# Optimization experiments

Measured on AMD Instinct MI355X. Metric: run time of the kernel, lower is better.

Reference implementation:

```python
import jax, jax.numpy as jnp
import numpy as np

DIM = 768
HEADS = 8
HEAD_DIM = DIM // HEADS  # 96, divisible by 6 for 3-axis RoPE
ROPE_BASE = 10000.0


def rotary_pe_3d(x, coords):
    """Apply 3D-coordinate rotary embedding.
    x: [B, h, L, d] with d % 6 == 0; coords: [B, L, 3].
    Head dim is split into 3 equal blocks, one per spatial axis; each block
    gets rotate-half RoPE with angle = coord_axis * inv_freq.
    """
    B, h, L, d = x.shape
    d3 = d // 3
    half = d3 // 2
    inv_freq = 1.0 / (ROPE_BASE ** (jnp.arange(half, dtype=x.dtype) / half))  # [half]
    ang = coords[..., None] * inv_freq  # [B, L, 3, half]
    cos = jnp.cos(ang)[:, None]  # [B, 1, L, 3, half]
    sin = jnp.sin(ang)[:, None]
    xr = x.reshape(B, h, L, 3, d3)
    x1, x2 = xr[..., :half], xr[..., half:]
    out = jnp.concatenate([x1 * cos - x2 * sin, x1 * sin + x2 * cos], axis=-1)
    return out.reshape(B, h, L, d)


def setup_inputs() -> dict:
    key = jax.random.key(0)
    ks = jax.random.split(key, 9)
    B, Lq, Lk = 2, 2048, 2048
    s = DIM ** -0.5
    return {
        "Q_in": jax.random.normal(ks[0], (B, Lq, DIM), jnp.float32),
        "K_in": jax.random.normal(ks[1], (B, Lk, DIM), jnp.float32),
        "V_in": jax.random.normal(ks[2], (B, Lk, DIM), jnp.float32),
        "coords_q": jax.random.uniform(ks[3], (B, Lq, 3), jnp.float32) * 10.0,
        "coords_k": jax.random.uniform(ks[4], (B, Lk, 3), jnp.float32) * 10.0,
        "Wq": jax.random.normal(ks[5], (DIM, DIM), jnp.float32) * s,
        "Wk": jax.random.normal(ks[6], (DIM, DIM), jnp.float32) * s,
        "Wv": jax.random.normal(ks[7], (DIM, DIM), jnp.float32) * s,
        "Wo": jax.random.normal(ks[8], (DIM, DIM), jnp.float32) * s,
    }


def _split_heads(x, h):
    B, L, C = x.shape
    return x.reshape(B, L, h, C // h).transpose(0, 2, 1, 3)  # [B,h,L,d]


def reference(Q_in, K_in, V_in, coords_q, coords_k, Wq, Wk, Wv, Wo):
    scale = HEAD_DIM ** -0.5
    q = _split_heads(Q_in @ Wq.T, HEADS)
    k = _split_heads(K_in @ Wk.T, HEADS)
    v = _split_heads(V_in @ Wv.T, HEADS)
    q = rotary_pe_3d(q, coords_q)
    k = rotary_pe_3d(k, coords_k)
    attn = jnp.einsum('bhqd,bhkd->bhqk', q, k) * scale
    attn = jax.nn.softmax(attn, axis=-1)
    out = jnp.einsum('bhqk,bhkd->bhqd', attn, v)
    B, h, L, d = out.shape
    out = out.transpose(0, 2, 1, 3).reshape(B, L, h * d)
    return out @ Wo.T
```

## Files before the change

kernel.cpp:

```cpp
#include <hip/hip_runtime.h>
#include <stdint.h>

#define H 8
#define DH 96
#define L 2048
#define NB 2
#define D 768

typedef unsigned short u16;
typedef unsigned int u32;
typedef __attribute__((ext_vector_type(4))) __bf16 bf16x4;
typedef __attribute__((ext_vector_type(8))) __bf16 bf16x8;
typedef __attribute__((ext_vector_type(4))) float f32x4;
typedef __attribute__((ext_vector_type(16))) float f32x16;
typedef __attribute__((ext_vector_type(4))) u32 u32x4;
typedef __attribute__((ext_vector_type(2))) u32 u32x2;
typedef __attribute__((ext_vector_type(4))) u16 u16x4;

#define QSCALE 0.14724444f

static __device__ __forceinline__ u16 f2bf(float f) {
  union { __bf16 h; u16 u; } v;
  v.h = (__bf16)f;
  return v.u;
}

static __device__ __forceinline__ bf16x8 cvt8r(f32x4 a, f32x4 b) {
  bf16x8 r;
  r[0] = (__bf16)a[0]; r[1] = (__bf16)a[1]; r[2] = (__bf16)a[2]; r[3] = (__bf16)a[3];
  r[4] = (__bf16)b[0]; r[5] = (__bf16)b[1]; r[6] = (__bf16)b[2]; r[7] = (__bf16)b[3];
  return r;
}

__global__ __launch_bounds__(256, 3)
void proj_qkv(const float* __restrict__ Qin, const float* __restrict__ Kin,
              const float* __restrict__ Vin,
              const float* __restrict__ Wq, const float* __restrict__ Wk,
              const float* __restrict__ Wv,
              const float* __restrict__ cq, const float* __restrict__ ck,
              u16* __restrict__ qo, u16* __restrict__ ko, u16* __restrict__ vo)
{
  __shared__ u16 a_lds[2][64 * 40];
  __shared__ u16 b_lds[2][192 * 40];
  const int tid = threadIdx.x;
  const int lane = tid & 63;
  const int w = tid >> 6;
  const int wr = w >> 1, wc = w & 1;
  const int fr = lane & 15;
  const int hi = lane >> 4;

  const int f = blockIdx.x;
  const int xcd = f & 7;
  const int g = f >> 3;
  const int bx = g & 3;
  const int h2 = g >> 2;
  const int byp = h2 & 7;
  const int z = h2 >> 3;
  const int by = xcd + 8 * byp;
  const int row0 = by * 64;
  const int col0 = bx * 192;

  const float* A = (z == 0) ? Qin : ((z == 1) ? Kin : Vin);
  const float* W = (z == 0) ? Wq : ((z == 1) ? Wk : Wv);

  const int arow = tid >> 2;
  const int acol = (tid & 3) * 8;
  const float* pA = A + (size_t)(row0 + arow) * D + acol;
  const float* pB0 = W + (size_t)(col0 + arow) * D + acol;
  const float* pB1 = pB0 + (size_t)64 * D;
  const float* pB2 = pB0 + (size_t)128 * D;

  f32x4 acc[2][6] = {};
  f32x4 Ra[2], Rb[6];

  auto issue = [&](int k) {
    Ra[0] = *(const f32x4*)(pA + k);
    Ra[1] = *(const f32x4*)(pA + k + 4);
    Rb[0] = *(const f32x4*)(pB0 + k);
    Rb[1] = *(const f32x4*)(pB0 + k + 4);
    Rb[2] = *(const f32x4*)(pB1 + k);
    Rb[3] = *(const f32x4*)(pB1 + k + 4);
    Rb[4] = *(const f32x4*)(pB2 + k);
    Rb[5] = *(const f32x4*)(pB2 + k + 4);
  };
  auto stage = [&](int bi) {
    *(bf16x8*)(&a_lds[bi][arow * 40 + acol]) = cvt8r(Ra[0], Ra[1]);
    *(bf16x8*)(&b_lds[bi][arow * 40 + acol]) = cvt8r(Rb[0], Rb[1]);
    *(bf16x8*)(&b_lds[bi][(arow + 64) * 40 + acol]) = cvt8r(Rb[2], Rb[3]);
    *(bf16x8*)(&b_lds[bi][(arow + 128) * 40 + acol]) = cvt8r(Rb[4], Rb[5]);
  };
  auto compute = [&](int bi) {
    bf16x8 af[2], bf[6];
#pragma unroll
    for (int m = 0; m < 2; m++)
      af[m] = *(const bf16x8*)(&a_lds[bi][(wr * 32 + m * 16 + fr) * 40 + hi * 8]);
#pragma unroll
    for (int n = 0; n < 6; n++)
      bf[n] = *(const bf16x8*)(&b_lds[bi][(wc * 96 + n * 16 + fr) * 40 + hi * 8]);
#pragma unroll
    for (int m = 0; m < 2; m++)
#pragma unroll
      for (int n = 0; n < 6; n++)
        acc[m][n] = __builtin_amdgcn_mfma_f32_16x16x32_bf16(af[m], bf[n], acc[m][n], 0, 0, 0);
  };

  issue(0);
  stage(0);
  __syncthreads();

  int cur = 0;
#pragma unroll 1
  for (int t = 0; t < 24; t++) {
    if (t + 1 < 24) issue((t + 1) * 32);
    compute(cur);
    if (t + 1 < 24) stage(cur ^ 1);
    __syncthreads();
    cur ^= 1;
  }

  const int hh = (col0 + wc * 96) / DH;
  if (z == 2) {
#pragma unroll
    for (int m = 0; m < 2; m++) {
      int rbase = row0 + wr * 32 + m * 16 + hi * 4;
#pragma unroll
      for (int n = 0; n < 6; n++) {
        int dd = n * 16 + fr;
#pragma unroll
        for (int r = 0; r < 4; r++) {
          int row = rbase + r;
          int b = row >> 11, l = row & (L - 1);
          vo[((size_t)((b * H + hh) * DH + dd)) * L + l] = f2bf(acc[m][n][r]);
        }
      }
    }
  } else {
    const float* coords = (z == 0) ? cq : ck;
    u16* outp = (z == 0) ? qo : ko;
    const float postscale = (z == 0) ? QSCALE : 1.0f;
    const float invf = exp2f(-(float)fr * 0.83048202372184058f);
#pragma unroll
    for (int m = 0; m < 2; m++) {
      int rbase = row0 + wr * 32 + m * 16 + hi * 4;
#pragma unroll
      for (int np = 0; np < 3; np++) {
        int n1 = np * 2;
        int dd1 = n1 * 16 + fr;
#pragma unroll
        for (int r = 0; r < 4; r++) {
          int row = rbase + r;
          int b = row >> 11, l = row & (L - 1);
          float coord = coords[((size_t)(b * L + l)) * 3 + np];
          float ang = coord * invf;
          float sn = __sinf(ang), cs = __cosf(ang);
          float x1 = acc[m][n1][r], x2 = acc[m][n1 + 1][r];
          size_t base = ((size_t)((b * H + hh) * L + l)) * DH;
          outp[base + dd1] = f2bf((x1 * cs - x2 * sn) * postscale);
          outp[base + dd1 + 16] = f2bf((x1 * sn + x2 * cs) * postscale);
        }
      }
    }
  }
}

#define KSTR 104
#define VSTR 76
#define NT   (L / 64)
__global__ __launch_bounds__(256, 2)
void attn_fwd(const u16* __restrict__ q_ws, const u16* __restrict__ k_ws,
              const u16* __restrict__ vt_ws, u16* __restrict__ ao)
{
  __shared__ __attribute__((aligned(16))) u16 k_lds[2][64 * KSTR];
  __shared__ __attribute__((aligned(16))) u16 vt_lds[2][96 * VSTR];
  const int tid = threadIdx.x;
  const int lane = tid & 63;
  const int w = tid >> 6;

  const int f = blockIdx.x;
  const int xr = f & 7;
  const int g = f >> 3;
  const int qx = g & 31;
  const int bh = xr + 8 * (g >> 5);
  const int q0 = qx * 64;

  const int qlo = lane & 31;
  const int hi32 = lane >> 5;
  const int wq = w >> 1;
  const int kk0 = (w & 1) * 32;

  const u16* kbase = k_ws + (size_t)bh * L * DH;
  const u16* vtbase = vt_ws + (size_t)bh * DH * L;

  const int perm[4] = {0, 2, 1, 3};

  int kg_off[3], kl0[3], kl1[3];
  int vg_off[3], vl0[3], vl1[3];
#pragma unroll
  for (int it = 0; it < 3; it++) {
    int ch = tid + it * 256;
    int krow = ch / 12, dc = ch % 12;
    kg_off[it] = krow * DH + dc * 8;
    int c0 = dc * 2;
    kl0[it] = krow * KSTR + (c0 >> 2) * 16 + perm[c0 & 3] * 4;
    kl1[it] = krow * KSTR + (c0 >> 2) * 16 + perm[(c0 + 1) & 3] * 4;
    int vrow = ch >> 3, vq = (ch & 7) * 2;
    vg_off[it] = vrow * L + vq * 4;
    vl0[it] = vrow * VSTR + (vq >> 2) * 16 + perm[vq & 3] * 4;
    vl1[it] = vrow * VSTR + (vq >> 2) * 16 + perm[(vq + 1) & 3] * 4;
  }

  bf16x8 qf[6];
  {
    const u16* qb = q_ws + ((size_t)bh * L + q0 + wq * 32 + qlo) * DH;
#pragma unroll
    for (int s = 0; s < 6; s++) {
      bf16x4 a = *(const bf16x4*)(qb + s * 16 + hi32 * 4);
      bf16x4 b = *(const bf16x4*)(qb + s * 16 + hi32 * 4 + 8);
      bf16x8 q;
      q[0] = a[0]; q[1] = a[1]; q[2] = a[2]; q[3] = a[3];
      q[4] = b[0]; q[5] = b[1]; q[6] = b[2]; q[7] = b[3];
      qf[s] = q;
    }
  }

  f32x16 o[3] = {};
  float m_r = -1e30f, l_r = 0.f;

  u32x4 kreg[3], vreg[3];
  auto kissue = [&](int t) {
    const u16* kb = kbase + (size_t)t * 64 * DH;
    const u16* vb = vtbase + t * 64;
#pragma unroll
    for (int it = 0; it < 3; it++) {
      kreg[it] = *(const u32x4*)(kb + kg_off[it]);
      vreg[it] = *(const u32x4*)(vb + vg_off[it]);
    }
  };
  auto kwrite = [&](int bi) {
#pragma unroll
    for (int it = 0; it < 3; it++) {
      u32x2 klo = { kreg[it][0], kreg[it][1] };
      u32x2 khi = { kreg[it][2], kreg[it][3] };
      *(u32x2*)(&k_lds[bi][kl0[it]]) = klo;
      *(u32x2*)(&k_lds[bi][kl1[it]]) = khi;
      u32x2 vlo = { vreg[it][0], vreg[it][1] };
      u32x2 vhi = { vreg[it][2], vreg[it][3] };
      *(u32x2*)(&vt_lds[bi][vl0[it]]) = vlo;
      *(u32x2*)(&vt_lds[bi][vl1[it]]) = vhi;
    }
  };

  kissue(0);
  kwrite(0);
  __syncthreads();

  int cur = 0;
  for (int t = 0; t < NT; t++) {
    if (t + 1 < NT) kissue(t + 1);

    f32x16 s2 = {};
#pragma unroll
    for (int s = 0; s < 6; s++) {
      bf16x8 kfrag = *(const bf16x8*)(
          &k_lds[cur][(kk0 + qlo) * KSTR + s * 16 + hi32 * 8]);
      s2 = __builtin_amdgcn_mfma_f32_32x32x16_bf16(kfrag, qf[s], s2, 0, 0, 0);
    }

    float a0 = fmaxf(fmaxf(s2[0], s2[1]), s2[2]);
    float a1 = fmaxf(fmaxf(s2[3], s2[4]), s2[5]);
    float a2 = fmaxf(fmaxf(s2[6], s2[7]), s2[8]);
    float a3 = fmaxf(fmaxf(s2[9], s2[10]), s2[11]);
    float a4 = fmaxf(fmaxf(s2[12], s2[13]), s2[14]);
    float pmax = fmaxf(fmaxf(fmaxf(a0, a1), a2), fmaxf(fmaxf(a3, a4), s2[15]));
    if (!__all(pmax - m_r <= 8.0f)) {
      float mx = fmaxf(pmax, __shfl_xor(pmax, 32));
      float mn = fmaxf(m_r, mx);
      float alpha = exp2f(m_r - mn);
      m_r = mn;
      l_r *= alpha;
#pragma unroll
      for (int db = 0; db < 3; db++)
#pragma unroll
        for (int r = 0; r < 16; r++)
          o[db][r] *= alpha;
    }

    float p[16];
    float rs = 0.f;
#pragma unroll
    for (int r = 0; r < 16; r++) {
      p[r] = exp2f(s2[r] - m_r);
      rs += p[r];
    }
    l_r += rs;

    bf16x8 pt[2];
#pragma unroll
    for (int s = 0; s < 2; s++)
#pragma unroll
      for (int j = 0; j < 8; j++)
        pt[s][j] = (__bf16)p[s * 8 + j];

#pragma unroll
    for (int s = 0; s < 2; s++)
#pragma unroll
      for (int db = 0; db < 3; db++) {
        bf16x8 vfrag = *(const bf16x8*)(
            &vt_lds[cur][(db * 32 + qlo) * VSTR + kk0 + s * 16 + hi32 * 8]);
        o[db] = __builtin_amdgcn_mfma_f32_32x32x16_bf16(vfrag, pt[s], o[db], 0, 0, 0);
      }

    if (t + 1 < NT) {
      kwrite(cur ^ 1);
      __syncthreads();
      cur ^= 1;
    }
  }

  float l_w = l_r + __shfl_xor(l_r, 32);

  {
    float* xb = (float*)&k_lds[wq][0];
    const int base = lane * 52;
    if (w & 1) {
#pragma unroll
      for (int db = 0; db < 3; db++)
#pragma unroll
        for (int rg = 0; rg < 4; rg++) {
          f32x4 v = { o[db][rg * 4], o[db][rg * 4 + 1],
                      o[db][rg * 4 + 2], o[db][rg * 4 + 3] };
          *(f32x4*)&xb[base + db * 16 + rg * 4] = v;
        }
      xb[base + 48] = m_r;
      xb[base + 49] = l_w;
    }
    __syncthreads();
    if (!(w & 1)) {
      float m1 = xb[base + 48], l1 = xb[base + 49];
      float ms = fmaxf(m_r, m1);
      float c0 = exp2f(m_r - ms), c1 = exp2f(m1 - ms);
      float inv = 1.f / (l_w * c0 + l1 * c1);
      const int b = bh >> 3, hh = bh & 7;
      const int lrow = q0 + wq * 32 + qlo;
      u16* aop = ao + ((size_t)(b * L + lrow)) * D + hh * DH;
#pragma unroll
      for (int db = 0; db < 3; db++)
#pragma unroll
        for (int rg = 0; rg < 4; rg++) {
          f32x4 op = *(const f32x4*)&xb[base + db * 16 + rg * 4];
          u16x4 pk;
#pragma unroll
          for (int r4 = 0; r4 < 4; r4++)
            pk[r4] = f2bf((o[db][rg * 4 + r4] * c0 + op[r4] * c1) * inv);
          *(u16x4*)(aop + db * 32 + rg * 8 + hi32 * 4) = pk;
        }
    }
  }
}

__global__ __launch_bounds__(256, 3)
void gemm_out(const u16* __restrict__ A, const float* __restrict__ W,
              float* __restrict__ out)
{
  __shared__ u16 a_lds[2][64 * 40];
  __shared__ u16 b_lds[2][64 * 40];
  const int tid = threadIdx.x;
  const int lane = tid & 63;
  const int w = tid >> 6;
  const int wr = w >> 1, wc = w & 1;

  const int f = blockIdx.x;
  const int xr = f & 7;
  const int g = f >> 3;
  const int bx = g % 12;
  const int wq = g / 12;
  const int by = xr + 8 * wq;
  const int row0 = by * 64;
  const int col0 = bx * 64;

  f32x4 acc[2][2] = {};
  const int srow = tid >> 2;
  const int scol = (tid & 3) * 8;
  const u16* pA = A + (size_t)(row0 + srow) * D + scol;
  const float* pW = W + (size_t)(col0 + srow) * D + scol;
  const int fr = lane & 15;
  const int fk = (lane >> 4) * 8;

  auto issueG = [&](int k, u32x4* ra, f32x4* rb) {
    ra[0] = *(const u32x4*)(pA + k);
    rb[0] = *(const f32x4*)(pW + k);
    rb[1] = *(const f32x4*)(pW + k + 4);
  };
  auto writeG = [&](int bi, const u32x4* ra, const f32x4* rb) {
    *(u32x4*)(&a_lds[bi][srow * 40 + scol]) = ra[0];
    *(bf16x8*)(&b_lds[bi][srow * 40 + scol]) = cvt8r(rb[0], rb[1]);
  };
  auto computeG = [&](int bi) {
    bf16x8 af[2], bfr[2];
#pragma unroll
    for (int m = 0; m < 2; m++)
      af[m] = *(const bf16x8*)(&a_lds[bi][(wr * 32 + m * 16 + fr) * 40 + fk]);
#pragma unroll
    for (int n = 0; n < 2; n++)
      bfr[n] = *(const bf16x8*)(&b_lds[bi][(wc * 32 + n * 16 + fr) * 40 + fk]);
#pragma unroll
    for (int m = 0; m < 2; m++)
#pragma unroll
      for (int n = 0; n < 2; n++)
        acc[m][n] = __builtin_amdgcn_mfma_f32_16x16x32_bf16(af[m], bfr[n], acc[m][n], 0, 0, 0);
  };

  u32x4 raA[1], raB[1];
  f32x4 rbA[2], rbB[2];
  issueG(0, raB, rbB);
  writeG(0, raB, rbB);
  issueG(32, raA, rbA);
  __syncthreads();

  for (int k0 = 0; k0 < D; k0 += 64) {
    if (k0 + 64 < D) issueG(k0 + 64, raB, rbB);
    computeG(0);
    writeG(1, raA, rbA);
    __syncthreads();
    if (k0 + 96 < D) issueG(k0 + 96, raA, rbA);
    computeG(1);
    if (k0 + 64 < D) writeG(0, raB, rbB);
    __syncthreads();
  }

#pragma unroll
  for (int m = 0; m < 2; m++) {
    int rbase = row0 + wr * 32 + m * 16 + (lane >> 4) * 4;
#pragma unroll
    for (int n = 0; n < 2; n++) {
      int c = col0 + wc * 32 + n * 16 + fr;
#pragma unroll
      for (int r = 0; r < 4; r++)
        out[(size_t)(rbase + r) * D + c] = acc[m][n][r];
    }
  }
}

extern "C" void kernel_launch(void* const* d_in, const int* in_sizes, int n_in,
                              void* d_out, int out_size, void* d_ws, size_t ws_size,
                              hipStream_t stream) {
  (void)in_sizes; (void)n_in; (void)out_size;
  const float* Qin = (const float*)d_in[0];
  const float* Kin = (const float*)d_in[1];
  const float* Vin = (const float*)d_in[2];
  const float* cq  = (const float*)d_in[3];
  const float* ck  = (const float*)d_in[4];
  const float* Wq  = (const float*)d_in[5];
  const float* Wk  = (const float*)d_in[6];
  const float* Wv  = (const float*)d_in[7];
  const float* Wo  = (const float*)d_in[8];
  float* out = (float*)d_out;

  const size_t per = (size_t)NB * H * L * DH;
  if (ws_size < 4 * per * sizeof(u16)) return;

  u16* q_ws  = (u16*)d_ws;
  u16* k_ws  = q_ws + per;
  u16* vt_ws = k_ws + per;
  u16* ao_ws = vt_ws + per;

  proj_qkv<<<dim3(768), dim3(256), 0, stream>>>(
      Qin, Kin, Vin, Wq, Wk, Wv, cq, ck, q_ws, k_ws, vt_ws);
  attn_fwd<<<dim3(32 * NB * H), dim3(256), 0, stream>>>(q_ws, k_ws, vt_ws, ao_ws);
  gemm_out<<<dim3(12 * 64), dim3(256), 0, stream>>>(ao_ws, Wo, out);
}
```

Measured before the change: 99.09 us.

## Rework attention to two waves each covering 64 query rows with DMA K loads

Measured after the change: 113.8 us. +14.8%, slower.

```diff
diff --git a/kernel.cpp b/kernel.cpp
--- a/kernel.cpp
+++ b/kernel.cpp
@@ -163,10 +163,10 @@
   }
 }
 
-#define KSTR 104
-#define VSTR 76
+#define KSTR 96
+#define VSTR 72
 #define NT   (L / 64)
-__global__ __launch_bounds__(256, 2)
+__global__ __launch_bounds__(128, 1)
 void attn_fwd(const u16* __restrict__ q_ws, const u16* __restrict__ k_ws,
               const u16* __restrict__ vt_ws, u16* __restrict__ ao)
 {
@@ -185,121 +185,148 @@
 
   const int qlo = lane & 31;
   const int hi32 = lane >> 5;
-  const int wq = w >> 1;
-  const int kk0 = (w & 1) * 32;
+  const int kk0 = w * 32;
 
   const u16* kbase = k_ws + (size_t)bh * L * DH;
   const u16* vtbase = vt_ws + (size_t)bh * DH * L;
 
   const int perm[4] = {0, 2, 1, 3};
 
-  int kg_off[3], kl0[3], kl1[3];
-  int vg_off[3], vl0[3], vl1[3];
-#pragma unroll
-  for (int it = 0; it < 3; it++) {
-    int ch = tid + it * 256;
-    int krow = ch / 12, dc = ch % 12;
-    kg_off[it] = krow * DH + dc * 8;
-    int c0 = dc * 2;
-    kl0[it] = krow * KSTR + (c0 >> 2) * 16 + perm[c0 & 3] * 4;
-    kl1[it] = krow * KSTR + (c0 >> 2) * 16 + perm[(c0 + 1) & 3] * 4;
+  int vg_off[6], vl0[6], vl1[6];
+#pragma unroll
+  for (int it = 0; it < 6; it++) {
+    int ch = tid + it * 128;
     int vrow = ch >> 3, vq = (ch & 7) * 2;
     vg_off[it] = vrow * L + vq * 4;
     vl0[it] = vrow * VSTR + (vq >> 2) * 16 + perm[vq & 3] * 4;
     vl1[it] = vrow * VSTR + (vq >> 2) * 16 + perm[(vq + 1) & 3] * 4;
   }
 
-  bf16x8 qf[6];
+  auto kdma = [&](int t, int bi) {
+#pragma unroll
+    for (int c = 0; c < 6; c++) {
+      const int blk = c * 2 + w;
+      const u16* gp = kbase + (size_t)t * 64 * DH + ((size_t)blk * 64 + lane) * 8;
+      u16* lp = &k_lds[bi][(size_t)blk * 512];
+      __builtin_amdgcn_global_load_lds(
+          (const __attribute__((address_space(1))) u32*)gp,
+          (__attribute__((address_space(3))) u32*)lp, 16, 0, 0);
+    }
+  };
+
+  bf16x8 qf[2][6];
   {
-    const u16* qb = q_ws + ((size_t)bh * L + q0 + wq * 32 + qlo) * DH;
+    const u16* qb0 = q_ws + ((size_t)bh * L + q0 + qlo) * DH;
+    const u16* qb1 = qb0 + (size_t)32 * DH;
 #pragma unroll
     for (int s = 0; s < 6; s++) {
-      bf16x4 a = *(const bf16x4*)(qb + s * 16 + hi32 * 4);
-      bf16x4 b = *(const bf16x4*)(qb + s * 16 + hi32 * 4 + 8);
-      bf16x8 q;
-      q[0] = a[0]; q[1] = a[1]; q[2] = a[2]; q[3] = a[3];
-      q[4] = b[0]; q[5] = b[1]; q[6] = b[2]; q[7] = b[3];
-      qf[s] = q;
-    }
-  }
-
-  f32x16 o[3] = {};
-  float m_r = -1e30f, l_r = 0.f;
-
-  u32x4 kreg[3], vreg[3];
-  auto kissue = [&](int t) {
-    const u16* kb = kbase + (size_t)t * 64 * DH;
+      qf[0][s] = *(const bf16x8*)(qb0 + s * 16 + hi32 * 8);
+      qf[1][s] = *(const bf16x8*)(qb1 + s * 16 + hi32 * 8);
+    }
+  }
+
+  f32x16 oA[3] = {}, oB[3] = {};
+  float mA = -1e30f, lA = 0.f, mB = -1e30f, lB = 0.f;
+
+  u32x4 vreg[6];
+  auto vissue = [&](int t) {
     const u16* vb = vtbase + t * 64;
 #pragma unroll
-    for (int it = 0; it < 3; it++) {
-      kreg[it] = *(const u32x4*)(kb + kg_off[it]);
+    for (int it = 0; it < 6; it++)
       vreg[it] = *(const u32x4*)(vb + vg_off[it]);
-    }
-  };
-  auto kwrite = [&](int bi) {
-#pragma unroll
-    for (int it = 0; it < 3; it++) {
-      u32x2 klo = { kreg[it][0], kreg[it][1] };
-      u32x2 khi = { kreg[it][2], kreg[it][3] };
-      *(u32x2*)(&k_lds[bi][kl0[it]]) = klo;
-      *(u32x2*)(&k_lds[bi][kl1[it]]) = khi;
-      u32x2 vlo = { vreg[it][0], vreg[it][1] };
-      u32x2 vhi = { vreg[it][2], vreg[it][3] };
-      *(u32x2*)(&vt_lds[bi][vl0[it]]) = vlo;
-      *(u32x2*)(&vt_lds[bi][vl1[it]]) = vhi;
-    }
-  };
-
-  kissue(0);
-  kwrite(0);
+  };
+  auto vwrite = [&](int bi) {
+#pragma unroll
+    for (int it = 0; it < 6; it++) {
+      u32x2 lo = { vreg[it][0], vreg[it][1] };
+      u32x2 hi2 = { vreg[it][2], vreg[it][3] };
+      *(u32x2*)(&vt_lds[bi][vl0[it]]) = lo;
+      *(u32x2*)(&vt_lds[bi][vl1[it]]) = hi2;
+    }
+  };
+
+  kdma(0, 0);
+  vissue(0);
+  vwrite(0);
   __syncthreads();
 
   int cur = 0;
   for (int t = 0; t < NT; t++) {
-    if (t + 1 < NT) kissue(t + 1);
-
-    f32x16 s2 = {};
+    if (t + 1 < NT) {
+      kdma(t + 1, cur ^ 1);
+      vissue(t + 1);
+    }
+
+    f32x16 sA = {}, sB = {};
 #pragma unroll
     for (int s = 0; s < 6; s++) {
       bf16x8 kfrag = *(const bf16x8*)(
           &k_lds[cur][(kk0 + qlo) * KSTR + s * 16 + hi32 * 8]);
-      s2 = __builtin_amdgcn_mfma_f32_32x32x16_bf16(kfrag, qf[s], s2, 0, 0, 0);
-    }
-
-    float a0 = fmaxf(fmaxf(s2[0], s2[1]), s2[2]);
-    float a1 = fmaxf(fmaxf(s2[3], s2[4]), s2[5]);
-    float a2 = fmaxf(fmaxf(s2[6], s2[7]), s2[8]);
-    float a3 = fmaxf(fmaxf(s2[9], s2[10]), s2[11]);
-    float a4 = fmaxf(fmaxf(s2[12], s2[13]), s2[14]);
-    float pmax = fmaxf(fmaxf(fmaxf(a0, a1), a2), fmaxf(fmaxf(a3, a4), s2[15]));
-    if (!__all(pmax - m_r <= 8.0f)) {
-      float mx = fmaxf(pmax, __shfl_xor(pmax, 32));
-      float mn = fmaxf(m_r, mx);
-      float alpha = exp2f(m_r - mn);
-      m_r = mn;
-      l_r *= alpha;
-#pragma unroll
-      for (int db = 0; db < 3; db++)
-#pragma unroll
-        for (int r = 0; r < 16; r++)
-          o[db][r] *= alpha;
-    }
-
-    float p[16];
-    float rs = 0.f;
-#pragma unroll
-    for (int r = 0; r < 16; r++) {
-      p[r] = exp2f(s2[r] - m_r);
-      rs += p[r];
-    }
-    l_r += rs;
-
-    bf16x8 pt[2];
-#pragma unroll
-    for (int s = 0; s < 2; s++)
-#pragma unroll
-      for (int j = 0; j < 8; j++)
-        pt[s][j] = (__bf16)p[s * 8 + j];
+      sA = __builtin_amdgcn_mfma_f32_32x32x16_bf16(kfrag, qf[0][s], sA, 0, 0, 0);
+      sB = __builtin_amdgcn_mfma_f32_32x32x16_bf16(kfrag, qf[1][s], sB, 0, 0, 0);
+    }
+
+    bf16x8 ptA[2], ptB[2];
+    {
+      float a0 = fmaxf(fmaxf(sA[0], sA[1]), sA[2]);
+      float a1 = fmaxf(fmaxf(sA[3], sA[4]), sA[5]);
+      float a2 = fmaxf(fmaxf(sA[6], sA[7]), sA[8]);
+      float a3 = fmaxf(fmaxf(sA[9], sA[10]), sA[11]);
+      float a4 = fmaxf(fmaxf(sA[12], sA[13]), sA[14]);
+      float pmax = fmaxf(fmaxf(fmaxf(a0, a1), a2), fmaxf(fmaxf(a3, a4), sA[15]));
+      if (!__all(pmax - mA <= 8.0f)) {
+        float mx = fmaxf(pmax, __shfl_xor(pmax, 32));
+        float mn = fmaxf(mA, mx);
+        float alpha = exp2f(mA - mn);
+        mA = mn;
+        lA *= alpha;
+#pragma unroll
+        for (int db = 0; db < 3; db++)
+#pragma unroll
+          for (int r = 0; r < 16; r++)
+            oA[db][r] *= alpha;
+      }
+      float p[16];
+      float rs = 0.f;
+#pragma unroll
+      for (int r = 0; r < 16; r++) { p[r] = exp2f(sA[r] - mA); rs += p[r]; }
+      lA += rs;
+#pragma unroll
+      for (int s = 0; s < 2; s++)
+#pragma unroll
+        for (int j = 0; j < 8; j++)
+          ptA[s][j] = (__bf16)p[s * 8 + j];
+    }
+    {
+      float a0 = fmaxf(fmaxf(sB[0], sB[1]), sB[2]);
+      float a1 = fmaxf(fmaxf(sB[3], sB[4]), sB[5]);
+      float a2 = fmaxf(fmaxf(sB[6], sB[7]), sB[8]);
+      float a3 = fmaxf(fmaxf(sB[9], sB[10]), sB[11]);
+      float a4 = fmaxf(fmaxf(sB[12], sB[13]), sB[14]);
+      float pmax = fmaxf(fmaxf(fmaxf(a0, a1), a2), fmaxf(fmaxf(a3, a4), sB[15]));
+      if (!__all(pmax - mB <= 8.0f)) {
+        float mx = fmaxf(pmax, __shfl_xor(pmax, 32));
+        float mn = fmaxf(mB, mx);
+        float alpha = exp2f(mB - mn);
+        mB = mn;
+        lB *= alpha;
+#pragma unroll
+        for (int db = 0; db < 3; db++)
+#pragma unroll
+          for (int r = 0; r < 16; r++)
+            oB[db][r] *= alpha;
+      }
+      float p[16];
+      float rs = 0.f;
+#pragma unroll
+      for (int r = 0; r < 16; r++) { p[r] = exp2f(sB[r] - mB); rs += p[r]; }
+      lB += rs;
+#pragma unroll
+      for (int s = 0; s < 2; s++)
+#pragma unroll
+        for (int j = 0; j < 8; j++)
+          ptB[s][j] = (__bf16)p[s * 8 + j];
+    }
 
 #pragma unroll
     for (int s = 0; s < 2; s++)
@@ -307,42 +334,67 @@
       for (int db = 0; db < 3; db++) {
         bf16x8 vfrag = *(const bf16x8*)(
             &vt_lds[cur][(db * 32 + qlo) * VSTR + kk0 + s * 16 + hi32 * 8]);
-        o[db] = __builtin_amdgcn_mfma_f32_32x32x16_bf16(vfrag, pt[s], o[db], 0, 0, 0);
+        oA[db] = __builtin_amdgcn_mfma_f32_32x32x16_bf16(vfrag, ptA[s], oA[db], 0, 0, 0);
+        oB[db] = __builtin_amdgcn_mfma_f32_32x32x16_bf16(vfrag, ptB[s], oB[db], 0, 0, 0);
       }
 
     if (t + 1 < NT) {
-      kwrite(cur ^ 1);
+      vwrite(cur ^ 1);
       __syncthreads();
       cur ^= 1;
     }
   }
 
-  float l_w = l_r + __shfl_xor(l_r, 32);
-
-  {
-    float* xb = (float*)&k_lds[wq][0];
-    const int base = lane * 52;
-    if (w & 1) {
+  float lAw = lA + __shfl_xor(lA, 32);
+  float lBw = lB + __shfl_xor(lB, 32);
+
+  __syncthreads();
+
+  float* xa = (float*)&k_lds[0][0];
+  float* xb = (float*)&vt_lds[0][0];
+  const int base = lane * 52;
+  if (w == 1) {
+#pragma unroll
+    for (int db = 0; db < 3; db++)
+#pragma unroll
+      for (int rg = 0; rg < 4; rg++) {
+        f32x4 va = { oA[db][rg * 4], oA[db][rg * 4 + 1],
+                     oA[db][rg * 4 + 2], oA[db][rg * 4 + 3] };
+        *(f32x4*)&xa[base + db * 16 + rg * 4] = va;
+        f32x4 vb = { oB[db][rg * 4], oB[db][rg * 4 + 1],
+                     oB[db][rg * 4 + 2], oB[db][rg * 4 + 3] };
+        *(f32x4*)&xb[base + db * 16 + rg * 4] = vb;
+      }
+    xa[base + 48] = mA; xa[base + 49] = lAw;
+    xb[base + 48] = mB; xb[base + 49] = lBw;
+  }
+  __syncthreads();
+  if (w == 0) {
+    const int b = bh >> 3, hh = bh & 7;
+    {
+      float m1 = xa[base + 48], l1 = xa[base + 49];
+      float ms = fmaxf(mA, m1);
+      float c0 = exp2f(mA - ms), c1 = exp2f(m1 - ms);
+      float inv = 1.f / (lAw * c0 + l1 * c1);
+      u16* aop = ao + ((size_t)(b * L + q0 + qlo)) * D + hh * DH;
 #pragma unroll
       for (int db = 0; db < 3; db++)
 #pragma unroll
         for (int rg = 0; rg < 4; rg++) {
-          f32x4 v = { o[db][rg * 4], o[db][rg * 4 + 1],
-                      o[db][rg * 4 + 2], o[db][rg * 4 + 3] };
-          *(f32x4*)&xb[base + db * 16 + rg * 4] = v;
+          f32x4 op = *(const f32x4*)&xa[base + db * 16 + rg * 4];
+          u16x4 pk;
+#pragma unroll
+          for (int r4 = 0; r4 < 4; r4++)
+            pk[r4] = f2bf((oA[db][rg * 4 + r4] * c0 + op[r4] * c1) * inv);
+          *(u16x4*)(aop + db * 32 + rg * 8 + hi32 * 4) = pk;
         }
-      xb[base + 48] = m_r;
-      xb[base + 49] = l_w;
-    }
-    __syncthreads();
-    if (!(w & 1)) {
+    }
+    {
       float m1 = xb[base + 48], l1 = xb[base + 49];
-      float ms = fmaxf(m_r, m1);
-      float c0 = exp2f(m_r - ms), c1 = exp2f(m1 - ms);
-      float inv = 1.f / (l_w * c0 + l1 * c1);
-      const int b = bh >> 3, hh = bh & 7;
-      const int lrow = q0 + wq * 32 + qlo;
-      u16* aop = ao + ((size_t)(b * L + lrow)) * D + hh * DH;
+      float ms = fmaxf(mB, m1);
+      float c0 = exp2f(mB - ms), c1 = exp2f(m1 - ms);
+      float inv = 1.f / (lBw * c0 + l1 * c1);
+      u16* aop = ao + ((size_t)(b * L + q0 + 32 + qlo)) * D + hh * DH;
 #pragma unroll
       for (int db = 0; db < 3; db++)
 #pragma unroll
@@ -351,7 +403,7 @@
           u16x4 pk;
 #pragma unroll
           for (int r4 = 0; r4 < 4; r4++)
-            pk[r4] = f2bf((o[db][rg * 4 + r4] * c0 + op[r4] * c1) * inv);
+            pk[r4] = f2bf((oB[db][rg * 4 + r4] * c0 + op[r4] * c1) * inv);
           *(u16x4*)(aop + db * 32 + rg * 8 + hi32 * 4) = pk;
         }
     }
@@ -466,6 +518,6 @@
 
   proj_qkv<<<dim3(768), dim3(256), 0, stream>>>(
       Qin, Kin, Vin, Wq, Wk, Wv, cq, ck, q_ws, k_ws, vt_ws);
-  attn_fwd<<<dim3(32 * NB * H), dim3(256), 0, stream>>>(q_ws, k_ws, vt_ws, ao_ws);
+  attn_fwd<<<dim3(32 * NB * H), dim3(128), 0, stream>>>(q_ws, k_ws, vt_ws, ao_ws);
   gemm_out<<<dim3(12 * 64), dim3(256), 0, stream>>>(ao_ws, Wo, out);
 }
```
